# Performance work log

Measured on AMD Instinct MI355X. Metric: run time of the kernel, lower is better.

The kernel has to match this reference:

```python
import jax, jax.numpy as jnp
import numpy as np

EPS = 1e-8  # torch cosine_similarity norm clamp
TEMP = 1.0

def _gelu(h):
    return jax.nn.gelu(h, approximate=False)  # torch nn.GELU default (erf)

def _layernorm(h, g, b, eps=1e-5):
    mu = jnp.mean(h, axis=-1, keepdims=True)
    var = jnp.var(h, axis=-1, keepdims=True)
    return (h - mu) * jax.lax.rsqrt(var + eps) * g + b

def _encoder(h, eW1, eb1, eW2, eb2, eW3, eb3, ln_g, ln_b):
    h = _gelu(h @ eW1 + eb1)
    h = _gelu(h @ eW2 + eb2)
    h = h @ eW3 + eb3
    return _layernorm(h, ln_g, ln_b)

def _normalize(v):
    n = jnp.sqrt(jnp.sum(v * v, axis=-1, keepdims=True))
    return v / jnp.maximum(n, EPS)

def setup_inputs() -> dict:
    key = jax.random.key(0)
    ks = jax.random.split(key, 8)
    B, D, H, K = 16384, 512, 512, 11
    s = 0.02
    return {
        'x': jax.random.normal(ks[0], (B, D), jnp.float32),
        'tW1': jax.random.normal(ks[1], (K, D, H), jnp.float32) * s,
        'tb1': jnp.zeros((K, H), jnp.float32),
        'tW2': jax.random.normal(ks[2], (K, H, H), jnp.float32) * s,
        'tb2': jnp.zeros((K, H), jnp.float32),
        'tW3': jax.random.normal(ks[3], (K, H, D), jnp.float32) * s,
        'tb3': jnp.zeros((K, D), jnp.float32),
        'eW1': jax.random.normal(ks[4], (D, H), jnp.float32) * s,
        'eb1': jnp.zeros((H,), jnp.float32),
        'eW2': jax.random.normal(ks[5], (H, H), jnp.float32) * s,
        'eb2': jnp.zeros((H,), jnp.float32),
        'eW3': jax.random.normal(ks[6], (H, H), jnp.float32) * s,
        'eb3': jnp.zeros((H,), jnp.float32),
        'ln_g': jnp.ones((H,), jnp.float32),
        'ln_b': jnp.zeros((H,), jnp.float32),
    }

def reference(x, tW1, tb1, tW2, tb2, tW3, tb3, eW1, eb1, eW2, eb2, eW3, eb3, ln_g, ln_b):
    K = tW1.shape[0]
    # K learned transforms, vectorized over k: [K, B, D]
    h = _gelu(jnp.einsum('bi,kij->kbj', x, tW1) + tb1[:, None, :])
    h = _gelu(jnp.einsum('kbi,kij->kbj', h, tW2) + tb2[:, None, :])
    tx = jnp.einsum('kbi,kij->kbj', h, tW3) + tb3[:, None, :]
    # shared encoder on x and on each transformed view
    z = _encoder(x, eW1, eb1, eW2, eb2, eW3, eb3, ln_g, ln_b)      # [B, H]
    zk = _encoder(tx, eW1, eb1, eW2, eb2, eW3, eb3, ln_g, ln_b)    # [K, B, H]
    zn = _normalize(z)
    zkn = _normalize(zk)
    pos = jnp.einsum('bh,kbh->kb', zn, zkn) / TEMP                 # sim(z, z_k)
    S = jnp.einsum('lbh,kbh->lkb', zkn, zkn) / TEMP                # sim(z_l, z_k)
    diag = jnp.eye(K, dtype=bool)[:, :, None]
    Sm = jnp.where(diag, -jnp.inf, S)                              # drop l == k
    all_terms = jnp.concatenate([pos[None], Sm], axis=0)           # [K+1, K, B]
    log_den = jax.nn.logsumexp(all_terms, axis=0)                  # [K, B]
    return -jnp.sum(pos - log_den, axis=0)                         # [B]
```

## Files before the change

kernel.cpp:

```cpp
#include <hip/hip_runtime.h>
#include <hip/hip_bf16.h>
#include <cstdint>

typedef __attribute__((ext_vector_type(8))) short short8;
typedef __attribute__((ext_vector_type(4))) float f32x4;
typedef __attribute__((ext_vector_type(4))) short short4v;

__device__ __forceinline__ float b2f(short s) {
    unsigned u = ((unsigned)(unsigned short)s) << 16;
    return __builtin_bit_cast(float, u);
}
__device__ __forceinline__ short f2b(float f) {
    unsigned u = __builtin_bit_cast(unsigned, f);
    u += 0x7fff + ((u >> 16) & 1);
    return (short)(u >> 16);
}

__device__ __forceinline__ float gelu_t(float x) {
    const float c1 = 2.302184829f;
    const float c2 = 0.102947246f;
    float x2 = x * x;
    float t  = __builtin_fmaf(c2, x2, c1);
    float e  = __builtin_amdgcn_exp2f(x * t);
    return x - __fdividef(x, e + 1.0f);
}

__device__ __forceinline__ void async16(const void* g, void* l) {
    __builtin_amdgcn_global_load_lds(
        (const __attribute__((address_space(1))) unsigned int*)g,
        (__attribute__((address_space(3))) unsigned int*)l, 16, 0, 0);
}

#define NT 16

template<bool GELU>
__global__ __launch_bounds__(512, 2)
void gemm_bt(const short* __restrict__ A, long sA,
             const short* __restrict__ Bt, long sB,
             const float* __restrict__ bias, long sBias,
             short* __restrict__ C, long sC) {
    const int z = blockIdx.z;
    A    += (long)z * sA;
    Bt   += (long)z * sB;
    bias += (long)z * sBias;
    C    += (long)z * sC;

    const int nwg = (int)gridDim.x;
    const int bx  = (int)blockIdx.x;
    int flat = bx;
    if ((nwg & 7) == 0) { const int q = nwg >> 3; flat = (bx & 7) * q + (bx >> 3); }
    const long arow0 = (long)(flat >> 1) * 256;
    const long brow0 = (long)(flat & 1) * 256;

    __shared__ alignas(16) short smem[3 * 16384];

    const int tid  = threadIdx.x;
    const int lane = tid & 63;
    const int w    = tid >> 6;
    const int wrow = w >> 2, wcol = w & 3;
    const int lr = lane & 15, hi = lane >> 4;

    f32x4 acc[8][4] = {};

    const int rl4 = lane >> 2;
    const int sc  = ((lane & 3) ^ (rl4 & 3)) * 8;

    auto stage = [&](int q, int t) {
        short* Ab = smem + q * 16384;
        short* Bb = Ab + 8192;
        const int k0 = t * 32;
#pragma unroll
        for (int j = 0; j < 2; ++j) {
            const int rbase = j * 128 + w * 16;
            async16(A  + (arow0 + rbase + rl4) * 512 + k0 + sc, Ab + rbase * 32);
            async16(Bt + (brow0 + rbase + rl4) * 512 + k0 + sc, Bb + rbase * 32);
        }
    };

    stage(0, 0);
    stage(1, 1);

#pragma unroll
    for (int t = 0; t < NT; ++t) {
        if (t + 2 < NT) stage((t + 2) % 3, t + 2);
        if (t + 2 < NT)      asm volatile("s_waitcnt vmcnt(8)" ::: "memory");
        else if (t + 1 < NT) asm volatile("s_waitcnt vmcnt(4)" ::: "memory");
        else                 asm volatile("s_waitcnt vmcnt(0)" ::: "memory");
        __builtin_amdgcn_sched_barrier(0);
        __builtin_amdgcn_s_barrier();
        __builtin_amdgcn_sched_barrier(0);

        const short* Ab = smem + (t % 3) * 16384;
        const short* Bb = Ab + 8192;
        short8 a[8], b[4];
#pragma unroll
        for (int n = 0; n < 4; ++n) {
            const int r = wcol * 64 + n * 16 + lr;
            b[n] = *(const short8*)&Bb[r * 32 + ((hi ^ (lr & 3)) * 8)];
        }
#pragma unroll
        for (int m = 0; m < 8; ++m) {
            const int r = wrow * 128 + m * 16 + lr;
            a[m] = *(const short8*)&Ab[r * 32 + ((hi ^ (lr & 3)) * 8)];
        }
#pragma unroll
        for (int m = 0; m < 8; ++m)
#pragma unroll
            for (int n = 0; n < 4; ++n)
                acc[m][n] = __builtin_amdgcn_mfma_f32_16x16x32_bf16(
                    a[m], b[n], acc[m][n], 0, 0, 0);

        __builtin_amdgcn_s_barrier();
    }

    short* E = smem + w * (32 * 72);
    const int cl = lr, rl = hi * 4;
#pragma unroll
    for (int h = 0; h < 4; ++h) {
#pragma unroll
        for (int n = 0; n < 4; ++n) {
            const int col = (int)brow0 + wcol * 64 + n * 16 + cl;
            const float bs = bias[col];
            const int ecol = n * 16 + cl;
#pragma unroll
            for (int ml = 0; ml < 2; ++ml) {
                const int m = h * 2 + ml;
                float g0 = acc[m][n][0] + bs, g1 = acc[m][n][1] + bs;
                float g2 = acc[m][n][2] + bs, g3 = acc[m][n][3] + bs;
                if (GELU) { g0 = gelu_t(g0); g1 = gelu_t(g1); g2 = gelu_t(g2); g3 = gelu_t(g3); }
                unsigned p01, p23;
                asm("v_cvt_pk_bf16_f32 %0, %1, %2" : "=v"(p01) : "v"(g0), "v"(g1));
                asm("v_cvt_pk_bf16_f32 %0, %1, %2" : "=v"(p23) : "v"(g2), "v"(g3));
                const int r0 = ml * 16 + rl;
                E[(r0 + 0) * 72 + ecol] = (short)(p01 & 0xffff);
                E[(r0 + 1) * 72 + ecol] = (short)(p01 >> 16);
                E[(r0 + 2) * 72 + ecol] = (short)(p23 & 0xffff);
                E[(r0 + 3) * 72 + ecol] = (short)(p23 >> 16);
            }
        }
#pragma unroll
        for (int chunk = 0; chunk < 4; ++chunk) {
            const int rloc = chunk * 8 + (lane >> 3);
            const int c0   = (lane & 7) * 8;
            short8 v = *(const short8*)&E[rloc * 72 + c0];
            *(short8*)&C[(arow0 + wrow * 128 + h * 32 + rloc) * 512
                         + brow0 + wcol * 64 + c0] = v;
        }
    }
}

__global__ __launch_bounds__(256)
void transpose_conv(const float* __restrict__ src, short* __restrict__ dst) {
    __shared__ float t[32][33];
    const long moff = (long)blockIdx.z * 512 * 512;
    const float* s = src + moff;
    short* d = dst + moff;
    const int tx = threadIdx.x & 31, ty = threadIdx.x >> 5;
    const int bi = blockIdx.x, bj = blockIdx.y;
#pragma unroll
    for (int j = 0; j < 4; ++j)
        t[ty + j * 8][tx] = s[(long)(bi * 32 + ty + j * 8) * 512 + bj * 32 + tx];
    __syncthreads();
#pragma unroll
    for (int j = 0; j < 4; ++j)
        d[(long)(bj * 32 + ty + j * 8) * 512 + bi * 32 + tx] = f2b(t[tx][ty + j * 8]);
}

__global__ __launch_bounds__(256)
void conv_f32_bf16_2(const float* __restrict__ src, short* __restrict__ d1,
                     short* __restrict__ d2, long n) {
    long i = ((long)blockIdx.x * 256 + threadIdx.x) * 4;
    if (i >= n) return;
    float4 f = *(const float4*)&src[i];
    short4v o;
    o[0] = f2b(f.x); o[1] = f2b(f.y); o[2] = f2b(f.z); o[3] = f2b(f.w);
    *(short4v*)&d1[i] = o;
    *(short4v*)&d2[i] = o;
}

__global__ __launch_bounds__(256)
void ln_loss(const short* __restrict__ H, const float* __restrict__ g,
             const float* __restrict__ bta, float* __restrict__ out, int CH) {
    __shared__ alignas(16) short Z[4][16 * 520];
    const int wid = threadIdx.x >> 6, lane = threadIdx.x & 63;
    const long b = (long)blockIdx.x * 4 + wid;
    short* Zw = &Z[wid][0];

#pragma unroll
    for (int r = 12; r < 16; ++r)
        *(short8*)&Zw[r * 520 + lane * 8] = (short8){0, 0, 0, 0, 0, 0, 0, 0};

    for (int s = 0; s < 12; ++s) {
        short8 t = *(const short8*)&H[((long)s * CH + b) * 512 + lane * 8];
        float v[8];
        float sum = 0.f, ss = 0.f;
#pragma unroll
        for (int j = 0; j < 8; ++j) { v[j] = b2f(t[j]); sum += v[j]; ss += v[j] * v[j]; }
#pragma unroll
        for (int o = 1; o < 64; o <<= 1) { sum += __shfl_xor(sum, o, 64); ss += __shfl_xor(ss, o, 64); }
        const float mu = sum * (1.f / 512.f);
        const float rs = rsqrtf(ss * (1.f / 512.f) - mu * mu + 1e-5f);
        float y[8]; float nsq = 0.f;
#pragma unroll
        for (int j = 0; j < 8; ++j) {
            const int col = lane * 8 + j;
            y[j] = (v[j] - mu) * rs * g[col] + bta[col];
            nsq += y[j] * y[j];
        }
#pragma unroll
        for (int o = 1; o < 64; o <<= 1) nsq += __shfl_xor(nsq, o, 64);
        const float inv = 1.f / fmaxf(sqrtf(nsq), 1e-8f);
        short8 o8;
#pragma unroll
        for (int j = 0; j < 8; ++j) o8[j] = f2b(y[j] * inv);
        *(short8*)&Zw[s * 520 + lane * 8] = o8;
    }

    f32x4 acc = {0.f, 0.f, 0.f, 0.f};
    const int lr = lane & 15, hi = lane >> 4;
#pragma unroll
    for (int st = 0; st < 16; ++st) {
        short8 a = *(const short8*)&Zw[lr * 520 + st * 32 + hi * 8];
        acc = __builtin_amdgcn_mfma_f32_16x16x32_bf16(a, a, acc, 0, 0, 0);
    }
    const int col = lr;
    float lmax = -3.0e38f;
    bool valid[4];
#pragma unroll
    for (int i = 0; i < 4; ++i) {
        const int row = hi * 4 + i;
        valid[i] = (row < 12) && (row != col);
        if (valid[i]) lmax = fmaxf(lmax, acc[i]);
    }
    lmax = fmaxf(lmax, __shfl_xor(lmax, 16, 64));
    lmax = fmaxf(lmax, __shfl_xor(lmax, 32, 64));
    float esum = 0.f;
#pragma unroll
    for (int i = 0; i < 4; ++i)
        if (valid[i]) esum += __builtin_amdgcn_exp2f((acc[i] - lmax) * 1.44269504f);
    esum += __shfl_xor(esum, 16, 64);
    esum += __shfl_xor(esum, 32, 64);
    float contrib = 0.f;
    if (hi == 0 && col >= 1 && col <= 11) {
        const float logden = lmax + __builtin_amdgcn_logf(esum) * 0.6931471806f;
        contrib = acc[0] - logden;
    }
#pragma unroll
    for (int o = 1; o < 16; o <<= 1) contrib += __shfl_xor(contrib, o, 64);
    if (lane == 0) out[b] = -contrib;
}

extern "C" void kernel_launch(void* const* d_in, const int* in_sizes, int n_in,
                              void* d_out, int out_size, void* d_ws, size_t ws_size,
                              hipStream_t stream) {
    const float* x    = (const float*)d_in[0];
    const float* tW1  = (const float*)d_in[1];
    const float* tb1  = (const float*)d_in[2];
    const float* tW2  = (const float*)d_in[3];
    const float* tb2  = (const float*)d_in[4];
    const float* tW3  = (const float*)d_in[5];
    const float* tb3  = (const float*)d_in[6];
    const float* eW1  = (const float*)d_in[7];
    const float* eb1  = (const float*)d_in[8];
    const float* eW2  = (const float*)d_in[9];
    const float* eb2  = (const float*)d_in[10];
    const float* eW3  = (const float*)d_in[11];
    const float* eb3  = (const float*)d_in[12];
    const float* ln_g = (const float*)d_in[13];
    const float* ln_b = (const float*)d_in[14];

    const int  B    = in_sizes[0] / 512;
    const long WMAT = 512L * 512L;

    int  c  = 1;
    long CH = B;
    for (;;) {
        CH = (long)B / c;
        size_t need = (size_t)36 * WMAT * 2 + (size_t)24 * CH * 512 * 2 + 4096;
        if (need <= ws_size || CH <= 256) break;
        c <<= 1;
    }
    const long SLAB = 12L * CH * 512;

    short* wt  = (short*)d_ws;
    short* X12 = wt  + 36L * WMAT;
    short* hA  = X12 + SLAB;

    {
        dim3 tgK(16, 16, 11), tg1(16, 16, 1);
        transpose_conv<<<tgK, 256, 0, stream>>>(tW1, wt + 0L * WMAT);
        transpose_conv<<<tgK, 256, 0, stream>>>(tW2, wt + 11L * WMAT);
        transpose_conv<<<tgK, 256, 0, stream>>>(tW3, wt + 22L * WMAT);
        transpose_conv<<<tg1, 256, 0, stream>>>(eW1, wt + 33L * WMAT);
        transpose_conv<<<tg1, 256, 0, stream>>>(eW2, wt + 34L * WMAT);
        transpose_conv<<<tg1, 256, 0, stream>>>(eW3, wt + 35L * WMAT);
    }

    const long SC = CH * 512;
    const dim3 gT((unsigned)(CH / 256 * 2), 1, 11);
    const dim3 gE((unsigned)(12 * CH / 256 * 2), 1, 1);

    for (int ch = 0; ch < c; ++ch) {
        conv_f32_bf16_2<<<(unsigned)((SC / 4 + 255) / 256), 256, 0, stream>>>(
            x + (long)ch * SC, X12, hA, SC);

        gemm_bt<true ><<<gT, 512, 0, stream>>>(hA,        0,  wt + 0L * WMAT,  WMAT, tb1, 512, X12 + SC, SC);
        gemm_bt<true ><<<gT, 512, 0, stream>>>(X12 + SC,  SC, wt + 11L * WMAT, WMAT, tb2, 512, hA + SC,  SC);
        gemm_bt<false><<<gT, 512, 0, stream>>>(hA + SC,   SC, wt + 22L * WMAT, WMAT, tb3, 512, X12 + SC, SC);

        gemm_bt<true ><<<gE, 512, 0, stream>>>(X12, 0, wt + 33L * WMAT, 0, eb1, 0, hA,  0);
        gemm_bt<true ><<<gE, 512, 0, stream>>>(hA,  0, wt + 34L * WMAT, 0, eb2, 0, X12, 0);
        gemm_bt<false><<<gE, 512, 0, stream>>>(X12, 0, wt + 35L * WMAT, 0, eb3, 0, hA,  0);

        ln_loss<<<(unsigned)(CH / 4), 256, 0, stream>>>(
            hA, ln_g, ln_b, (float*)d_out + (long)ch * CH, (int)CH);
    }
}
```

Measured before the change: 1.054 ms.

## Switch GEMM mainloop to BK=64 double-buffered pipeline with 8-wide swizzle

The GEMM mainloop now takes K-tiles of 64 instead of 32, so there are half as many iterations and barriers. The 3-stage LDS ring becomes a 2-stage double buffer, and the XOR swizzle is widened to 8 chunks to match the 64-element rows. MFMA sections are wrapped in s_setprio to favour the math waves. LDS use rises from 96KB to 128KB per block, which could hurt the 2-blocks-per-CU occupancy, and prefetch depth drops to one stage.

```diff
diff --git a/kernel.cpp b/kernel.cpp
--- a/kernel.cpp
+++ b/kernel.cpp
@@ -31,7 +31,7 @@
         (__attribute__((address_space(3))) unsigned int*)l, 16, 0, 0);
 }
 
-#define NT 16
+#define NT 8
 
 template<bool GELU>
 __global__ __launch_bounds__(512, 2)
@@ -52,7 +52,7 @@
     const long arow0 = (long)(flat >> 1) * 256;
     const long brow0 = (long)(flat & 1) * 256;
 
-    __shared__ alignas(16) short smem[3 * 16384];
+    __shared__ alignas(16) short smem[2 * 2 * 256 * 64];
 
     const int tid  = threadIdx.x;
     const int lane = tid & 63;
@@ -62,55 +62,64 @@
 
     f32x4 acc[8][4] = {};
 
-    const int rl4 = lane >> 2;
-    const int sc  = ((lane & 3) ^ (rl4 & 3)) * 8;
+    const int srow = lane >> 3;
+    const int sc   = ((lane & 7) ^ srow) * 8;
 
     auto stage = [&](int q, int t) {
-        short* Ab = smem + q * 16384;
-        short* Bb = Ab + 8192;
-        const int k0 = t * 32;
-#pragma unroll
-        for (int j = 0; j < 2; ++j) {
-            const int rbase = j * 128 + w * 16;
-            async16(A  + (arow0 + rbase + rl4) * 512 + k0 + sc, Ab + rbase * 32);
-            async16(Bt + (brow0 + rbase + rl4) * 512 + k0 + sc, Bb + rbase * 32);
+        short* Ab = smem + q * 32768;
+        short* Bb = Ab + 16384;
+        const int k0 = t * 64;
+#pragma unroll
+        for (int j = 0; j < 4; ++j) {
+            const int rbase = j * 64 + w * 8;
+            async16(A  + (arow0 + rbase + srow) * 512 + k0 + sc, Ab + rbase * 64);
+            async16(Bt + (brow0 + rbase + srow) * 512 + k0 + sc, Bb + rbase * 64);
         }
     };
 
     stage(0, 0);
-    stage(1, 1);
-
+
+    int buf = 0;
 #pragma unroll
     for (int t = 0; t < NT; ++t) {
-        if (t + 2 < NT) stage((t + 2) % 3, t + 2);
-        if (t + 2 < NT)      asm volatile("s_waitcnt vmcnt(8)" ::: "memory");
-        else if (t + 1 < NT) asm volatile("s_waitcnt vmcnt(4)" ::: "memory");
-        else                 asm volatile("s_waitcnt vmcnt(0)" ::: "memory");
+        if (t + 1 < NT) {
+            stage(buf ^ 1, t + 1);
+            asm volatile("s_waitcnt vmcnt(8)" ::: "memory");
+        } else {
+            asm volatile("s_waitcnt vmcnt(0)" ::: "memory");
+        }
         __builtin_amdgcn_sched_barrier(0);
         __builtin_amdgcn_s_barrier();
         __builtin_amdgcn_sched_barrier(0);
 
-        const short* Ab = smem + (t % 3) * 16384;
-        const short* Bb = Ab + 8192;
-        short8 a[8], b[4];
-#pragma unroll
-        for (int n = 0; n < 4; ++n) {
-            const int r = wcol * 64 + n * 16 + lr;
-            b[n] = *(const short8*)&Bb[r * 32 + ((hi ^ (lr & 3)) * 8)];
-        }
-#pragma unroll
-        for (int m = 0; m < 8; ++m) {
-            const int r = wrow * 128 + m * 16 + lr;
-            a[m] = *(const short8*)&Ab[r * 32 + ((hi ^ (lr & 3)) * 8)];
-        }
-#pragma unroll
-        for (int m = 0; m < 8; ++m)
-#pragma unroll
-            for (int n = 0; n < 4; ++n)
-                acc[m][n] = __builtin_amdgcn_mfma_f32_16x16x32_bf16(
-                    a[m], b[n], acc[m][n], 0, 0, 0);
+        const short* Ab = smem + buf * 32768;
+        const short* Bb = Ab + 16384;
+#pragma unroll
+        for (int ks = 0; ks < 2; ++ks) {
+            const int ch = ks * 4 + hi;
+            short8 a[8], b[4];
+#pragma unroll
+            for (int n = 0; n < 4; ++n) {
+                const int r = wcol * 64 + n * 16 + lr;
+                b[n] = *(const short8*)&Bb[r * 64 + ((ch ^ (r & 7)) * 8)];
+            }
+#pragma unroll
+            for (int m = 0; m < 8; ++m) {
+                const int r = wrow * 128 + m * 16 + lr;
+                a[m] = *(const short8*)&Ab[r * 64 + ((ch ^ (r & 7)) * 8)];
+            }
+            __builtin_amdgcn_s_setprio(1);
+#pragma unroll
+            for (int m = 0; m < 8; ++m)
+#pragma unroll
+                for (int n = 0; n < 4; ++n)
+                    acc[m][n] = __builtin_amdgcn_mfma_f32_16x16x32_bf16(
+                        a[m], b[n], acc[m][n], 0, 0, 0);
+            __builtin_amdgcn_s_setprio(0);
+        }
 
         __builtin_amdgcn_s_barrier();
+        buf ^= 1;
     }
 
     short* E = smem + w * (32 * 72);
```

Measured after the change: 1.001 ms. 1.05x faster.
